# Kernel tuning notes

Hardware: AMD Instinct MI355X
Metric: run time of the kernel (lower is better)

Reference implementation:

```python
import jax, jax.numpy as jnp
import numpy as np

E = 2048  # embedding_size; must equal seq_len for the original assignment to be shape-valid
B = 64    # batch


def setup_inputs() -> dict:
    key = jax.random.key(0)
    # tokens must lie in dictionary = {1, ..., E-1}; otherwise the original code drops rows
    x = jax.random.randint(key, (B, E), 1, E, dtype=jnp.int32)
    return {"x": x}


def reference(x):
    # Original per-token encoding: (m-1) leading '0's + bin(v) + trailing '1'
    # == big-endian E-bit binary representation of (2*v + 1).
    # Due to the transposed slice assignment, Y[j, b, i] = bit (E-1-b) of (2*x[i,j]+1).
    v = (2 * x + 1).astype(jnp.int32)                     # [B, J]
    shifts = E - 1 - jnp.arange(E, dtype=jnp.int32)       # bit index for output column b
    safe = jnp.minimum(shifts, 31)                        # v is nonneg, so v>>31 == 0 (correct high bits)
    bits = (v[:, :, None] >> safe[None, None, :]) & 1     # [B, J, E]
    return jnp.transpose(bits, (1, 2, 0)).astype(jnp.float32)  # Y: [J, E, B] == [seq, emb, batch]
```

## Files before the change

kernel.cpp:

```cpp
#include <hip/hip_runtime.h>


#define EMB 2048
#define BATCH 64

__global__ __launch_bounds__(256) void emb_bits_kernel(
    const int* __restrict__ x, float4* __restrict__ out) {
    unsigned int q  = blockIdx.x * 256u + threadIdx.x;
    unsigned int i4 = q & 15u;
    unsigned int jb = q >> 4;
    unsigned int b  = jb & 2047u;
    unsigned int j  = jb >> 11;
    int shift = 2047 - (int)b;

    float4 val = make_float4(0.f, 0.f, 0.f, 0.f);
    if (shift <= 11) {
        unsigned int i0 = i4 * 4u;
        int v0 = 2 * x[(i0 + 0) * EMB + j] + 1;
        int v1 = 2 * x[(i0 + 1) * EMB + j] + 1;
        int v2 = 2 * x[(i0 + 2) * EMB + j] + 1;
        int v3 = 2 * x[(i0 + 3) * EMB + j] + 1;
        val.x = (float)((v0 >> shift) & 1);
        val.y = (float)((v1 >> shift) & 1);
        val.z = (float)((v2 >> shift) & 1);
        val.w = (float)((v3 >> shift) & 1);
    }
    out[q] = val;
}

extern "C" void kernel_launch(void* const* d_in, const int* in_sizes, int n_in,
                              void* d_out, int out_size, void* d_ws, size_t ws_size,
                              hipStream_t stream) {
    const int* x = (const int*)d_in[0];
    float4* out = (float4*)d_out;
    const unsigned int quads = (unsigned int)EMB * EMB * BATCH / 4u;
    dim3 grid(quads / 256u);
    emb_bits_kernel<<<grid, dim3(256), 0, stream>>>(x, out);
}
```

Measured before the change: 1.025 ms.

## Use grid-stride loop with fixed 2048 blocks and per-thread uniform branch

```diff
diff --git a/kernel.cpp b/kernel.cpp
--- a/kernel.cpp
+++ b/kernel.cpp
@@ -3,29 +3,46 @@
 
 #define EMB 2048
 #define BATCH 64
+#define NBLOCKS 2048
+#define NTHREADS (NBLOCKS * 256u)
+#define NQUADS   ((unsigned int)EMB * EMB * BATCH / 4u)
+#define ITERS    (NQUADS / NTHREADS)
 
 __global__ __launch_bounds__(256) void emb_bits_kernel(
     const int* __restrict__ x, float4* __restrict__ out) {
-    unsigned int q  = blockIdx.x * 256u + threadIdx.x;
-    unsigned int i4 = q & 15u;
-    unsigned int jb = q >> 4;
+    unsigned int t  = blockIdx.x * 256u + threadIdx.x;
+    unsigned int i4 = t & 15u;
+    unsigned int jb = t >> 4;
     unsigned int b  = jb & 2047u;
-    unsigned int j  = jb >> 11;
+    unsigned int j0 = jb >> 11;
     int shift = 2047 - (int)b;
 
-    float4 val = make_float4(0.f, 0.f, 0.f, 0.f);
-    if (shift <= 11) {
+    float4* p = out + t;
+    if (shift > 11) {
+        const float4 z = make_float4(0.f, 0.f, 0.f, 0.f);
+        #pragma unroll 8
+        for (unsigned int it = 0; it < ITERS; ++it) {
+            *p = z;
+            p += NTHREADS;
+        }
+    } else {
         unsigned int i0 = i4 * 4u;
-        int v0 = 2 * x[(i0 + 0) * EMB + j] + 1;
-        int v1 = 2 * x[(i0 + 1) * EMB + j] + 1;
-        int v2 = 2 * x[(i0 + 2) * EMB + j] + 1;
-        int v3 = 2 * x[(i0 + 3) * EMB + j] + 1;
-        val.x = (float)((v0 >> shift) & 1);
-        val.y = (float)((v1 >> shift) & 1);
-        val.z = (float)((v2 >> shift) & 1);
-        val.w = (float)((v3 >> shift) & 1);
+        #pragma unroll 2
+        for (unsigned int it = 0; it < ITERS; ++it) {
+            unsigned int j = j0 + (it << 4);
+            int v0 = 2 * x[(i0 + 0) * EMB + j] + 1;
+            int v1 = 2 * x[(i0 + 1) * EMB + j] + 1;
+            int v2 = 2 * x[(i0 + 2) * EMB + j] + 1;
+            int v3 = 2 * x[(i0 + 3) * EMB + j] + 1;
+            float4 val;
+            val.x = (float)((v0 >> shift) & 1);
+            val.y = (float)((v1 >> shift) & 1);
+            val.z = (float)((v2 >> shift) & 1);
+            val.w = (float)((v3 >> shift) & 1);
+            *p = val;
+            p += NTHREADS;
+        }
     }
-    out[q] = val;
 }
 
 extern "C" void kernel_launch(void* const* d_in, const int* in_sizes, int n_in,
@@ -33,7 +50,5 @@
                               hipStream_t stream) {
     const int* x = (const int*)d_in[0];
     float4* out = (float4*)d_out;
-    const unsigned int quads = (unsigned int)EMB * EMB * BATCH / 4u;
-    dim3 grid(quads / 256u);
-    emb_bits_kernel<<<grid, dim3(256), 0, stream>>>(x, out);
+    emb_bits_kernel<<<dim3(NBLOCKS), dim3(256), 0, stream>>>(x, out);
 }
```

Result: slower. 1.341 ms (+30.9%).
